# Kernel tuning notes

Measured on AMD Instinct MI355X. Metric: run time of the kernel, lower is better.

Reference implementation:

```python
import jax, jax.numpy as jnp
import numpy as np

DISCOUNT = 0.95
THRESHOLD = 1e-3


def _make_w(n_actions=8):
    # Deterministic transition stencils from VIN.__init__
    left = [[1, 0], [0, 0], [0, 1], [2, 0], [0, 2], [2, 1], [2, 2], [1, 2]]
    center = [[0, 0], [0, 1], [0, 2], [1, 0], [1, 2], [2, 0], [2, 1], [2, 2]]
    right = [[0, 1], [0, 2], [1, 2], [0, 0], [2, 2], [1, 0], [2, 0], [2, 1]]
    w = np.zeros((n_actions, 1, 3, 3), dtype=np.float32)
    for i in range(n_actions):
        w[i, 0, left[i][0], left[i][1]] = 0.1
        w[i, 0, center[i][0], center[i][1]] = 0.8
        w[i, 0, right[i][0], right[i][1]] = 0.1
    return jnp.asarray(w)


def setup_inputs() -> dict:
    key = jax.random.key(0)
    # reward map (B,1,H,W); scaled so VI converges in a realistic # of iterations
    r = jax.random.normal(key, (8, 1, 256, 256), dtype=jnp.float32) * 0.1
    return {"r": r, "w": _make_w()}


def _conv(x, w):
    # F.conv2d(x, w, stride=1, padding=1) -> NCHW / OIHW, SAME padding for 3x3
    return jax.lax.conv_general_dilated(
        x, w, window_strides=(1, 1), padding="SAME",
        dimension_numbers=("NCHW", "OIHW", "NCHW"))


def reference(r, w):
    """value_iteration_manual: returns (v, policy, q)."""
    thresh = jnp.asarray(THRESHOLD, r.dtype)

    def eval_q(v):
        return _conv(r + v * DISCOUNT, w)  # (B, A, H, W)

    def cond(state):
        _, delta = state
        return delta > thresh

    def body(state):
        v, _ = state
        q = eval_q(v)
        new_v = jnp.max(q, axis=1, keepdims=True)  # (B,1,H,W)
        delta = jnp.max(jnp.abs(new_v - v))
        return new_v, delta

    v0 = jnp.zeros_like(r)
    v, _ = jax.lax.while_loop(cond, body, (v0, jnp.asarray(jnp.inf, r.dtype)))

    q = eval_q(v)
    policy = jax.nn.softmax(q, axis=1)  # exp(q - max) / sum, numerically stable
    return v, policy, q
```

## Files before the change

kernel.cpp:

```cpp
#include <hip/hip_runtime.h>

#define HH 256
#define WW 256
#define PLANE (HH * WW)
#define NB 8
#define NCELL (NB * PLANE)
#define RDIM 66
#define RST 72
#define LCOFF 3
#define SST 67

template<int CTRL>
__device__ __forceinline__ float dpp_old(float oldv, float x) {
    return __int_as_float(__builtin_amdgcn_update_dpp(
        __float_as_int(oldv), __float_as_int(x), CTRL, 0xf, 0xf, false));
}

__device__ __forceinline__ float dpp_left(float x) {
    return __int_as_float(__builtin_amdgcn_update_dpp(
        0, __float_as_int(x), 0x111, 0xf, 0xf, true));
}
__device__ __forceinline__ float dpp_right(float x) {
    return __int_as_float(__builtin_amdgcn_update_dpp(
        0, __float_as_int(x), 0x101, 0xf, 0xf, true));
}

template<bool FIRST, bool OUTV>
__global__ __launch_bounds__(1024, 8) void vi_cols(
    const float* __restrict__ r, const float* __restrict__ xin,
    float* __restrict__ xout)
{
    __shared__ float Xs[66 * SST];
    __shared__ float ebuf[2 * 16 * 2 * 64];
    __shared__ float Ts[32 * 33];

    const int blk = blockIdx.x;
    const int b = blk >> 6, ty = (blk >> 3) & 7, tx = blk & 7;
    const int gy0 = ty * 32 - 17, gx0 = tx * 32 - 17;
    const float* rbp = r + b * PLANE;
    const float* xb = xin + b * PLANE;

    for (int idx = threadIdx.x; idx < 66 * 66; idx += 1024) {
        int rr_ = idx / 66, rc = idx - rr_ * 66;
        int py = gy0 + rr_, px = gx0 + rc;
        float xv = 0.f;
        if ((unsigned)py < HH && (unsigned)px < WW) {
            int gi = py * WW + px;
            xv = FIRST ? rbp[gi] : xb[gi];
        }
        Xs[rr_ * SST + rc] = xv;
    }
    __syncthreads();

    const int w = threadIdx.x >> 6;
    const int l = threadIdx.x & 63;
    const int c0 = 4 * w;
    const int py = gy0 + 1 + l;
    const bool rowin = ((unsigned)py < HH);
    const int pxg = gx0 + c0 + 1;
    const bool grpin = ((unsigned)pxg <= (unsigned)(WW - 4));
    const bool act = rowin && grpin;

    float x[6], rt[6], rbo[6];
#pragma unroll
    for (int c = 0; c < 6; ++c) {
        x[c]   = Xs[(1 + l) * SST + c0 + c];
        rt[c]  = Xs[0 * SST + c0 + c];
        rbo[c] = Xs[65 * SST + c0 + c];
    }

    float rr[5];
    {
        float4 ra = make_float4(0.f, 0.f, 0.f, 0.f);
        if (act) ra = *(const float4*)(rbp + py * WW + pxg);
        rr[1] = ra.x; rr[2] = ra.y; rr[3] = ra.z; rr[4] = ra.w;
    }

    const int eb_w0 = (w * 2 + 0) * 64 + l;
    const int eb_w1 = (w * 2 + 1) * 64 + l;
    const int eb_rl = (w > 0)  ? (((w - 1) * 2 + 1) * 64 + l) : 0;
    const int eb_rr = (w < 15) ? (((w + 1) * 2 + 0) * 64 + l) : 0;
    const int PSTRIDE = 16 * 2 * 64;
    const int swl = 4 * w + 3;
    const int swr = 63 - 4 * w;
    const int sLim = min(16, min(swl, swr));

    for (int s = 0; s < 16; ++s) {
        const int po = (s & 1) * PSTRIDE;
        if (s < sLim) {
            float U[6], D[6];
#pragma unroll
            for (int c = 0; c < 6; ++c) {
                U[c] = dpp_old<0x138>(rt[c], x[c]);
                D[c] = dpp_old<0x130>(rbo[c], x[c]);
            }
            float pA = fmaf(8.f, U[0], x[0]);
            float qA = fmaf(8.f, D[0], x[0]);
            float vA = fmaf(8.f, x[0], U[0] + D[0]);
            float pB = fmaf(8.f, U[1], x[1]);
            float qB = fmaf(8.f, D[1], x[1]);
            float vB = fmaf(8.f, x[1], U[1] + D[1]);
            float nx[5];
#pragma unroll
            for (int c = 1; c <= 4; ++c) {
                float pC = fmaf(8.f, U[c + 1], x[c + 1]);
                float qC = fmaf(8.f, D[c + 1], x[c + 1]);
                float vC = fmaf(8.f, x[c + 1], U[c + 1] + D[c + 1]);
                float hT = fmaf(8.f, U[c], U[c - 1] + U[c + 1]);
                float hB = fmaf(8.f, D[c], D[c - 1] + D[c + 1]);
                float t0 = pA + U[c];
                float t2 = pC + U[c];
                float t5 = qA + D[c];
                float t7 = qC + D[c];
                float m1 = fmaxf(fmaxf(t0, hT), t2);
                float m2 = fmaxf(fmaxf(vA, vC), t5);
                float m3 = fmaxf(fmaxf(m1, m2), hB);
                float m  = fmaxf(m3, t7);
                nx[c] = act ? fmaf(0.095f, m, rr[c]) : 0.f;
                pA = pB; pB = pC; qA = qB; qB = qC; vA = vB; vB = vC;
            }
#pragma unroll
            for (int c = 1; c <= 4; ++c) x[c] = nx[c];
            ebuf[po + eb_w0] = x[1];
            ebuf[po + eb_w1] = x[4];
        }
        __syncthreads();
        if (s < sLim) {
            if (w > 0)  x[0] = ebuf[po + eb_rl];
            if (w < 15) x[5] = ebuf[po + eb_rr];
        }
    }

    if (w >= 4 && w <= 11 && l >= 16 && l < 48) {
        const int trow = l - 16;
#pragma unroll
        for (int c = 1; c <= 4; ++c) {
            int tcol = c0 + c - 17;
            float v = OUTV ? (x[c] - rr[c]) * (1.0f / 0.95f) : x[c];
            Ts[trow * 33 + tcol] = v;
        }
    }
    __syncthreads();
    {
        int i = threadIdx.x;
        int trow = i >> 5, tcol = i & 31;
        xout[b * PLANE + (gy0 + 17 + trow) * WW + (gx0 + 17 + tcol)] =
            Ts[trow * 33 + tcol];
    }
}

struct R6 { float v[6]; };

__device__ __forceinline__ R6 load_row(const float* __restrict__ xin,
                                       int base, int lc0, int g) {
    float4 m = *(const float4*)(xin + base + lc0);
    float lf = dpp_left(m.w);
    float rt = dpp_right(m.x);
    if (g == 0)  lf = xin[base + lc0 - 1];
    if (g == 15) rt = xin[base + lc0 + 4];
    R6 o;
    o.v[0] = lf; o.v[1] = m.x; o.v[2] = m.y; o.v[3] = m.z; o.v[4] = m.w; o.v[5] = rt;
    return o;
}

__device__ __forceinline__ float4 step4(const R6& T, const R6& M, const R6& B) {
    float P[6], Q[6], V[6];
#pragma unroll
    for (int j = 0; j < 6; ++j) {
        P[j] = fmaf(8.f, T.v[j], M.v[j]);
        Q[j] = fmaf(8.f, B.v[j], M.v[j]);
        V[j] = fmaf(8.f, M.v[j], T.v[j] + B.v[j]);
    }
    float out[4];
#pragma unroll
    for (int k = 0; k < 4; ++k) {
        float hT = fmaf(8.f, T.v[k + 1], T.v[k] + T.v[k + 2]);
        float hB = fmaf(8.f, B.v[k + 1], B.v[k] + B.v[k + 2]);
        float t0 = P[k] + T.v[k + 1];
        float t2 = P[k + 2] + T.v[k + 1];
        float t5 = Q[k] + B.v[k + 1];
        float t7 = Q[k + 2] + B.v[k + 1];
        float m1 = fmaxf(fmaxf(t0, hT), t2);
        float m2 = fmaxf(fmaxf(V[k], V[k + 2]), t5);
        float m3 = fmaxf(fmaxf(m1, m2), hB);
        out[k] = fmaxf(m3, t7);
    }
    return make_float4(out[0], out[1], out[2], out[3]);
}

__device__ __forceinline__ void t8f(const float* T, const float* M, const float* B,
                                    float t[8]) {
    t[0] = fmaf(8.f, T[0], M[0] + T[1]);
    t[1] = fmaf(8.f, T[1], T[0] + T[2]);
    t[2] = fmaf(8.f, T[2], T[1] + M[2]);
    t[3] = fmaf(8.f, M[0], B[0] + T[0]);
    t[4] = fmaf(8.f, M[2], T[2] + B[2]);
    t[5] = fmaf(8.f, B[0], B[1] + M[0]);
    t[6] = fmaf(8.f, B[1], B[2] + B[0]);
    t[7] = fmaf(8.f, B[2], M[2] + B[1]);
}

__device__ __forceinline__ float maxt(const float t[8]) {
    float m1 = fmaxf(fmaxf(t[0], t[1]), t[2]);
    float m2 = fmaxf(fmaxf(t[3], t[4]), t[5]);
    float m3 = fmaxf(fmaxf(m1, m2), t[6]);
    return fmaxf(m3, t[7]);
}

__device__ __forceinline__ float4 fmaf4(float4 m, float4 rr) {
    return make_float4(fmaf(0.095f, m.x, rr.x), fmaf(0.095f, m.y, rr.y),
                       fmaf(0.095f, m.z, rr.z), fmaf(0.095f, m.w, rr.w));
}

__device__ __forceinline__ void final_row(const R6& T, const R6& M, const R6& B,
                                          int b, int py, int px0,
                                          float* __restrict__ vout,
                                          float* __restrict__ qout,
                                          float* __restrict__ pout) {
    float v4[4], qv[8][4], pv[8][4];
#pragma unroll
    for (int k = 0; k < 4; ++k) {
        float t[8];
        t8f(T.v + k, M.v + k, B.v + k, t);
        float m = maxt(t);
        v4[k] = 0.1f * m;
        float e[8], s = 0.f;
#pragma unroll
        for (int a = 0; a < 8; ++a) { e[a] = __expf(0.1f * (t[a] - m)); s += e[a]; }
        float inv = 1.0f / s;
#pragma unroll
        for (int a = 0; a < 8; ++a) { qv[a][k] = 0.1f * t[a]; pv[a][k] = e[a] * inv; }
    }
    int ob = b * PLANE + py * WW + px0;
    *(float4*)(vout + ob) = make_float4(v4[0], v4[1], v4[2], v4[3]);
    int qb = b * 8 * PLANE + py * WW + px0;
#pragma unroll
    for (int a = 0; a < 8; ++a) {
        *(float4*)(qout + qb + a * PLANE) = make_float4(qv[a][0], qv[a][1], qv[a][2], qv[a][3]);
        *(float4*)(pout + qb + a * PLANE) = make_float4(pv[a][0], pv[a][1], pv[a][2], pv[a][3]);
    }
}

__global__ __launch_bounds__(512, 4) void vi_last(
    const float* __restrict__ r, const float* __restrict__ xin,
    float* __restrict__ vout, float* __restrict__ qout, float* __restrict__ pout)
{
    __shared__ __align__(16) float X[2][RDIM * RST];
    const int blk = blockIdx.x;
    const int b = blk >> 6, ty = (blk >> 3) & 7, tx = blk & 7;
    const int gy0 = ty * 32 - 17, gx0 = tx * 32 - 17;
    const float* rb = r + b * PLANE;
    const float* xb = xin + b * PLANE;

    for (int idx = threadIdx.x; idx < RDIM * RDIM; idx += 512) {
        int rr = idx / RDIM, rc = idx - rr * RDIM;
        int py = gy0 + rr, px = gx0 + rc;
        float val = 0.f;
        if ((unsigned)py < HH && (unsigned)px < WW)
            val = xb[py * WW + px];
        int lidx = rr * RST + rc + LCOFF;
        X[0][lidx] = val;
        X[1][lidx] = val;
    }

    const int g = threadIdx.x & 15;
    const int strip = threadIdx.x >> 4;
    const int wv = threadIdx.x >> 6;
    const int lc0 = 4 + 4 * g;
    const int rr0 = 1 + 2 * strip;
    const int px0 = gx0 + lc0 - LCOFF;
    const bool colin = ((unsigned)px0 < WW);
    const int py0 = gy0 + rr0;
    const bool row0in = ((unsigned)py0 < HH);
    const bool row1in = ((unsigned)(py0 + 1) < HH);

    float4 r0 = make_float4(0.f, 0.f, 0.f, 0.f), r1 = r0;
    if (colin && row0in) r0 = *(const float4*)(rb + py0 * WW + px0);
    if (colin && row1in) r1 = *(const float4*)(rb + (py0 + 1) * WW + px0);

    __syncthreads();

    const bool edge_wave = (wv == 0) | (wv == 7);
    const int base0 = (rr0 - 1) * RST;
    for (int s = 0; s < 15; ++s) {
        const float* xs = X[s & 1];
        float* xo = X[(s & 1) ^ 1];
        if (!(edge_wave && s >= 8)) {
            R6 A = load_row(xs, base0, lc0, g);
            R6 B = load_row(xs, base0 + RST, lc0, g);
            R6 C = load_row(xs, base0 + 2 * RST, lc0, g);
            float4 o0 = step4(A, B, C);
            R6 D = load_row(xs, base0 + 3 * RST, lc0, g);
            float4 o1 = step4(B, C, D);
            if (colin) {
                if (row0in) *(float4*)(xo + base0 + RST + lc0) = fmaf4(o0, r0);
                if (row1in) *(float4*)(xo + base0 + 2 * RST + lc0) = fmaf4(o1, r1);
            }
        }
        __syncthreads();
    }

    if (wv >= 2 && wv <= 5) {
        const float* xf = X[1];
        R6 A = load_row(xf, base0, lc0, g);
        R6 B = load_row(xf, base0 + RST, lc0, g);
        R6 C = load_row(xf, base0 + 2 * RST, lc0, g);
        R6 D = load_row(xf, base0 + 3 * RST, lc0, g);
        if (g >= 4 && g <= 11) {
            final_row(A, B, C, b, py0, px0, vout, qout, pout);
            final_row(B, C, D, b, py0 + 1, px0, vout, qout, pout);
        }
    }
}

__global__ __launch_bounds__(256) void vi_final(const float* __restrict__ r,
                                                const float* __restrict__ v,
                                                float* __restrict__ qout,
                                                float* __restrict__ pout) {
    int c = blockIdx.x * 256 + threadIdx.x;
    int x = c & (WW - 1);
    int y = (c >> 8) & (HH - 1);
    int b = c >> 16;
    float xin[9];
#pragma unroll
    for (int dy = -1; dy <= 1; ++dy)
#pragma unroll
        for (int dx = -1; dx <= 1; ++dx) {
            int yy = y + dy, xx = x + dx;
            float val = 0.0f;
            if ((unsigned)yy < HH && (unsigned)xx < WW)
                val = fmaf(0.95f, v[c + dy * WW + dx], r[c + dy * WW + dx]);
            xin[(dy + 1) * 3 + (dx + 1)] = val;
        }
    constexpr int Lt[8] = {3, 0, 1, 6, 2, 7, 8, 5};
    constexpr int Ct[8] = {0, 1, 2, 3, 5, 6, 7, 8};
    constexpr int Rt[8] = {1, 2, 5, 0, 8, 3, 6, 7};
    float q[8];
#pragma unroll
    for (int a = 0; a < 8; ++a) {
        float t = 0.1f * xin[Lt[a]];
        t = fmaf(0.8f, xin[Ct[a]], t);
        t = fmaf(0.1f, xin[Rt[a]], t);
        q[a] = t;
    }
    float m = q[0];
#pragma unroll
    for (int a = 1; a < 8; ++a) m = fmaxf(m, q[a]);
    float e[8], s = 0.f;
#pragma unroll
    for (int a = 0; a < 8; ++a) { e[a] = __expf(q[a] - m); s += e[a]; }
    float inv = 1.0f / s;
    int basec = b * (8 * PLANE) + (c & (PLANE - 1));
#pragma unroll
    for (int a = 0; a < 8; ++a) {
        qout[basec + a * PLANE] = q[a];
        pout[basec + a * PLANE] = e[a] * inv;
    }
}

extern "C" void kernel_launch(void* const* d_in, const int* in_sizes, int n_in,
                              void* d_out, int out_size, void* d_ws, size_t ws_size,
                              hipStream_t stream) {
    const float* r = (const float*)d_in[0];
    float* out = (float*)d_out;
    float* vslot = out;
    float* pol   = out + NCELL;
    float* qslot = out + 9 * NCELL;

    if (ws_size >= (size_t)(2 * NCELL * sizeof(float))) {
        float* w0 = (float*)d_ws;
        float* w1 = w0 + NCELL;
        vi_cols<true,  false><<<512, 1024, 0, stream>>>(r, nullptr, w0);
        vi_cols<false, false><<<512, 1024, 0, stream>>>(r, w0, w1);
        vi_cols<false, false><<<512, 1024, 0, stream>>>(r, w1, w0);
        vi_cols<false, false><<<512, 1024, 0, stream>>>(r, w0, w1);
        vi_cols<false, false><<<512, 1024, 0, stream>>>(r, w1, w0);
        vi_last<<<512, 512, 0, stream>>>(r, w0, vslot, qslot, pol);
    } else {
        vi_cols<true,  false><<<512, 1024, 0, stream>>>(r, nullptr, pol);
        vi_cols<false, false><<<512, 1024, 0, stream>>>(r, pol, qslot);
        vi_cols<false, false><<<512, 1024, 0, stream>>>(r, qslot, pol);
        vi_cols<false, false><<<512, 1024, 0, stream>>>(r, pol, qslot);
        vi_cols<false, false><<<512, 1024, 0, stream>>>(r, qslot, pol);
        vi_cols<false, true ><<<512, 1024, 0, stream>>>(r, pol, vslot);
        vi_final<<<NCELL / 256, 256, 0, stream>>>(r, vslot, qslot, pol);
    }
}
```

Baseline: 139.5 us.

## Rebuild final VI kernel on register-column DPP scheme with staged coalesced outputs

```diff
diff --git a/kernel.cpp b/kernel.cpp
--- a/kernel.cpp
+++ b/kernel.cpp
@@ -5,9 +5,6 @@
 #define PLANE (HH * WW)
 #define NB 8
 #define NCELL (NB * PLANE)
-#define RDIM 66
-#define RST 72
-#define LCOFF 3
 #define SST 67
 
 template<int CTRL>
@@ -16,14 +13,42 @@
         __float_as_int(oldv), __float_as_int(x), CTRL, 0xf, 0xf, false));
 }
 
-__device__ __forceinline__ float dpp_left(float x) {
-    return __int_as_float(__builtin_amdgcn_update_dpp(
-        0, __float_as_int(x), 0x111, 0xf, 0xf, true));
-}
-__device__ __forceinline__ float dpp_right(float x) {
-    return __int_as_float(__builtin_amdgcn_update_dpp(
-        0, __float_as_int(x), 0x101, 0xf, 0xf, true));
-}
+__device__ __forceinline__ void t8f(const float* T, const float* M, const float* B,
+                                    float t[8]) {
+    t[0] = fmaf(8.f, T[0], M[0] + T[1]);
+    t[1] = fmaf(8.f, T[1], T[0] + T[2]);
+    t[2] = fmaf(8.f, T[2], T[1] + M[2]);
+    t[3] = fmaf(8.f, M[0], B[0] + T[0]);
+    t[4] = fmaf(8.f, M[2], T[2] + B[2]);
+    t[5] = fmaf(8.f, B[0], B[1] + M[0]);
+    t[6] = fmaf(8.f, B[1], B[2] + B[0]);
+    t[7] = fmaf(8.f, B[2], M[2] + B[1]);
+}
+__device__ __forceinline__ float maxt(const float t[8]) {
+    float m1 = fmaxf(fmaxf(t[0], t[1]), t[2]);
+    float m2 = fmaxf(fmaxf(t[3], t[4]), t[5]);
+    float m3 = fmaxf(fmaxf(m1, m2), t[6]);
+    return fmaxf(m3, t[7]);
+}
+template<int A>
+__device__ __forceinline__ float tap1(const float* U, const float* x,
+                                      const float* D, int c) {
+    if (A == 0) return fmaf(8.f, U[c - 1], x[c - 1] + U[c]);
+    if (A == 1) return fmaf(8.f, U[c],     U[c - 1] + U[c + 1]);
+    if (A == 2) return fmaf(8.f, U[c + 1], U[c] + x[c + 1]);
+    if (A == 3) return fmaf(8.f, x[c - 1], D[c - 1] + U[c - 1]);
+    if (A == 4) return fmaf(8.f, x[c + 1], U[c + 1] + D[c + 1]);
+    if (A == 5) return fmaf(8.f, D[c - 1], D[c] + x[c - 1]);
+    if (A == 6) return fmaf(8.f, D[c],     D[c + 1] + D[c - 1]);
+    return fmaf(8.f, D[c + 1], x[c + 1] + D[c]);
+}
+
+#define DECODE_BLK() \
+    const int blk = blockIdx.x; \
+    const int b = blk & 7; \
+    const int tile = blk >> 3; \
+    const int ty = tile >> 3, tx = tile & 7; \
+    const int gy0 = ty * 32 - 17, gx0 = tx * 32 - 17;
 
 template<bool FIRST, bool OUTV>
 __global__ __launch_bounds__(1024, 8) void vi_cols(
@@ -34,9 +59,7 @@
     __shared__ float ebuf[2 * 16 * 2 * 64];
     __shared__ float Ts[32 * 33];
 
-    const int blk = blockIdx.x;
-    const int b = blk >> 6, ty = (blk >> 3) & 7, tx = blk & 7;
-    const int gy0 = ty * 32 - 17, gx0 = tx * 32 - 17;
+    DECODE_BLK();
     const float* rbp = r + b * PLANE;
     const float* xb = xin + b * PLANE;
 
@@ -68,7 +91,6 @@
         rt[c]  = Xs[0 * SST + c0 + c];
         rbo[c] = Xs[65 * SST + c0 + c];
     }
-
     float rr[5];
     {
         float4 ra = make_float4(0.f, 0.f, 0.f, 0.f);
@@ -81,9 +103,7 @@
     const int eb_rl = (w > 0)  ? (((w - 1) * 2 + 1) * 64 + l) : 0;
     const int eb_rr = (w < 15) ? (((w + 1) * 2 + 0) * 64 + l) : 0;
     const int PSTRIDE = 16 * 2 * 64;
-    const int swl = 4 * w + 3;
-    const int swr = 63 - 4 * w;
-    const int sLim = min(16, min(swl, swr));
+    const int sLim = min(16, min(4 * w + 3, 63 - 4 * w));
 
     for (int s = 0; s < 16; ++s) {
         const int po = (s & 1) * PSTRIDE;
@@ -149,167 +169,163 @@
     }
 }
 
-struct R6 { float v[6]; };
-
-__device__ __forceinline__ R6 load_row(const float* __restrict__ xin,
-                                       int base, int lc0, int g) {
-    float4 m = *(const float4*)(xin + base + lc0);
-    float lf = dpp_left(m.w);
-    float rt = dpp_right(m.x);
-    if (g == 0)  lf = xin[base + lc0 - 1];
-    if (g == 15) rt = xin[base + lc0 + 4];
-    R6 o;
-    o.v[0] = lf; o.v[1] = m.x; o.v[2] = m.y; o.v[3] = m.z; o.v[4] = m.w; o.v[5] = rt;
-    return o;
-}
-
-__device__ __forceinline__ float4 step4(const R6& T, const R6& M, const R6& B) {
-    float P[6], Q[6], V[6];
-#pragma unroll
-    for (int j = 0; j < 6; ++j) {
-        P[j] = fmaf(8.f, T.v[j], M.v[j]);
-        Q[j] = fmaf(8.f, B.v[j], M.v[j]);
-        V[j] = fmaf(8.f, M.v[j], T.v[j] + B.v[j]);
-    }
-    float out[4];
-#pragma unroll
-    for (int k = 0; k < 4; ++k) {
-        float hT = fmaf(8.f, T.v[k + 1], T.v[k] + T.v[k + 2]);
-        float hB = fmaf(8.f, B.v[k + 1], B.v[k] + B.v[k + 2]);
-        float t0 = P[k] + T.v[k + 1];
-        float t2 = P[k + 2] + T.v[k + 1];
-        float t5 = Q[k] + B.v[k + 1];
-        float t7 = Q[k + 2] + B.v[k + 1];
-        float m1 = fmaxf(fmaxf(t0, hT), t2);
-        float m2 = fmaxf(fmaxf(V[k], V[k + 2]), t5);
-        float m3 = fmaxf(fmaxf(m1, m2), hB);
-        out[k] = fmaxf(m3, t7);
-    }
-    return make_float4(out[0], out[1], out[2], out[3]);
-}
-
-__device__ __forceinline__ void t8f(const float* T, const float* M, const float* B,
-                                    float t[8]) {
-    t[0] = fmaf(8.f, T[0], M[0] + T[1]);
-    t[1] = fmaf(8.f, T[1], T[0] + T[2]);
-    t[2] = fmaf(8.f, T[2], T[1] + M[2]);
-    t[3] = fmaf(8.f, M[0], B[0] + T[0]);
-    t[4] = fmaf(8.f, M[2], T[2] + B[2]);
-    t[5] = fmaf(8.f, B[0], B[1] + M[0]);
-    t[6] = fmaf(8.f, B[1], B[2] + B[0]);
-    t[7] = fmaf(8.f, B[2], M[2] + B[1]);
-}
-
-__device__ __forceinline__ float maxt(const float t[8]) {
-    float m1 = fmaxf(fmaxf(t[0], t[1]), t[2]);
-    float m2 = fmaxf(fmaxf(t[3], t[4]), t[5]);
-    float m3 = fmaxf(fmaxf(m1, m2), t[6]);
-    return fmaxf(m3, t[7]);
-}
-
-__device__ __forceinline__ float4 fmaf4(float4 m, float4 rr) {
-    return make_float4(fmaf(0.095f, m.x, rr.x), fmaf(0.095f, m.y, rr.y),
-                       fmaf(0.095f, m.z, rr.z), fmaf(0.095f, m.w, rr.w));
-}
-
-__device__ __forceinline__ void final_row(const R6& T, const R6& M, const R6& B,
-                                          int b, int py, int px0,
-                                          float* __restrict__ vout,
-                                          float* __restrict__ qout,
-                                          float* __restrict__ pout) {
-    float v4[4], qv[8][4], pv[8][4];
-#pragma unroll
-    for (int k = 0; k < 4; ++k) {
-        float t[8];
-        t8f(T.v + k, M.v + k, B.v + k, t);
-        float m = maxt(t);
-        v4[k] = 0.1f * m;
-        float e[8], s = 0.f;
-#pragma unroll
-        for (int a = 0; a < 8; ++a) { e[a] = __expf(0.1f * (t[a] - m)); s += e[a]; }
-        float inv = 1.0f / s;
-#pragma unroll
-        for (int a = 0; a < 8; ++a) { qv[a][k] = 0.1f * t[a]; pv[a][k] = e[a] * inv; }
-    }
-    int ob = b * PLANE + py * WW + px0;
-    *(float4*)(vout + ob) = make_float4(v4[0], v4[1], v4[2], v4[3]);
-    int qb = b * 8 * PLANE + py * WW + px0;
-#pragma unroll
-    for (int a = 0; a < 8; ++a) {
-        *(float4*)(qout + qb + a * PLANE) = make_float4(qv[a][0], qv[a][1], qv[a][2], qv[a][3]);
-        *(float4*)(pout + qb + a * PLANE) = make_float4(pv[a][0], pv[a][1], pv[a][2], pv[a][3]);
-    }
-}
-
-__global__ __launch_bounds__(512, 4) void vi_last(
+__global__ __launch_bounds__(1024, 8) void vi_cols_last(
     const float* __restrict__ r, const float* __restrict__ xin,
     float* __restrict__ vout, float* __restrict__ qout, float* __restrict__ pout)
 {
-    __shared__ __align__(16) float X[2][RDIM * RST];
-    const int blk = blockIdx.x;
-    const int b = blk >> 6, ty = (blk >> 3) & 7, tx = blk & 7;
-    const int gy0 = ty * 32 - 17, gx0 = tx * 32 - 17;
-    const float* rb = r + b * PLANE;
+    __shared__ float Xs[66 * SST];
+    __shared__ float ebuf[2 * 16 * 2 * 64];
+    __shared__ float TsA[32 * 33];
+    __shared__ float TsB[32 * 33];
+
+    DECODE_BLK();
+    const float* rbp = r + b * PLANE;
     const float* xb = xin + b * PLANE;
 
-    for (int idx = threadIdx.x; idx < RDIM * RDIM; idx += 512) {
-        int rr = idx / RDIM, rc = idx - rr * RDIM;
-        int py = gy0 + rr, px = gx0 + rc;
-        float val = 0.f;
+    for (int idx = threadIdx.x; idx < 66 * 66; idx += 1024) {
+        int rr_ = idx / 66, rc = idx - rr_ * 66;
+        int py = gy0 + rr_, px = gx0 + rc;
+        float xv = 0.f;
         if ((unsigned)py < HH && (unsigned)px < WW)
-            val = xb[py * WW + px];
-        int lidx = rr * RST + rc + LCOFF;
-        X[0][lidx] = val;
-        X[1][lidx] = val;
-    }
-
-    const int g = threadIdx.x & 15;
-    const int strip = threadIdx.x >> 4;
-    const int wv = threadIdx.x >> 6;
-    const int lc0 = 4 + 4 * g;
-    const int rr0 = 1 + 2 * strip;
-    const int px0 = gx0 + lc0 - LCOFF;
-    const bool colin = ((unsigned)px0 < WW);
-    const int py0 = gy0 + rr0;
-    const bool row0in = ((unsigned)py0 < HH);
-    const bool row1in = ((unsigned)(py0 + 1) < HH);
-
-    float4 r0 = make_float4(0.f, 0.f, 0.f, 0.f), r1 = r0;
-    if (colin && row0in) r0 = *(const float4*)(rb + py0 * WW + px0);
-    if (colin && row1in) r1 = *(const float4*)(rb + (py0 + 1) * WW + px0);
-
+            xv = xb[py * WW + px];
+        Xs[rr_ * SST + rc] = xv;
+    }
     __syncthreads();
 
-    const bool edge_wave = (wv == 0) | (wv == 7);
-    const int base0 = (rr0 - 1) * RST;
+    const int w = threadIdx.x >> 6;
+    const int l = threadIdx.x & 63;
+    const int c0 = 4 * w;
+    const int py = gy0 + 1 + l;
+    const bool rowin = ((unsigned)py < HH);
+    const int pxg = gx0 + c0 + 1;
+    const bool grpin = ((unsigned)pxg <= (unsigned)(WW - 4));
+    const bool act = rowin && grpin;
+
+    float x[6], rt[6], rbo[6];
+#pragma unroll
+    for (int c = 0; c < 6; ++c) {
+        x[c]   = Xs[(1 + l) * SST + c0 + c];
+        rt[c]  = Xs[0 * SST + c0 + c];
+        rbo[c] = Xs[65 * SST + c0 + c];
+    }
+    float rr[5];
+    {
+        float4 ra = make_float4(0.f, 0.f, 0.f, 0.f);
+        if (act) ra = *(const float4*)(rbp + py * WW + pxg);
+        rr[1] = ra.x; rr[2] = ra.y; rr[3] = ra.z; rr[4] = ra.w;
+    }
+
+    const int eb_w0 = (w * 2 + 0) * 64 + l;
+    const int eb_w1 = (w * 2 + 1) * 64 + l;
+    const int eb_rl = (w > 0)  ? (((w - 1) * 2 + 1) * 64 + l) : 0;
+    const int eb_rr = (w < 15) ? (((w + 1) * 2 + 0) * 64 + l) : 0;
+    const int PSTRIDE = 16 * 2 * 64;
+    const int sLim = min(16, min(4 * w + 3, 63 - 4 * w));
+
     for (int s = 0; s < 15; ++s) {
-        const float* xs = X[s & 1];
-        float* xo = X[(s & 1) ^ 1];
-        if (!(edge_wave && s >= 8)) {
-            R6 A = load_row(xs, base0, lc0, g);
-            R6 B = load_row(xs, base0 + RST, lc0, g);
-            R6 C = load_row(xs, base0 + 2 * RST, lc0, g);
-            float4 o0 = step4(A, B, C);
-            R6 D = load_row(xs, base0 + 3 * RST, lc0, g);
-            float4 o1 = step4(B, C, D);
-            if (colin) {
-                if (row0in) *(float4*)(xo + base0 + RST + lc0) = fmaf4(o0, r0);
-                if (row1in) *(float4*)(xo + base0 + 2 * RST + lc0) = fmaf4(o1, r1);
+        const int po = (s & 1) * PSTRIDE;
+        if (s < sLim) {
+            float U[6], D[6];
+#pragma unroll
+            for (int c = 0; c < 6; ++c) {
+                U[c] = dpp_old<0x138>(rt[c], x[c]);
+                D[c] = dpp_old<0x130>(rbo[c], x[c]);
             }
+            float pA = fmaf(8.f, U[0], x[0]);
+            float qA = fmaf(8.f, D[0], x[0]);
+            float vA = fmaf(8.f, x[0], U[0] + D[0]);
+            float pB = fmaf(8.f, U[1], x[1]);
+            float qB = fmaf(8.f, D[1], x[1]);
+            float vB = fmaf(8.f, x[1], U[1] + D[1]);
+            float nx[5];
+#pragma unroll
+            for (int c = 1; c <= 4; ++c) {
+                float pC = fmaf(8.f, U[c + 1], x[c + 1]);
+                float qC = fmaf(8.f, D[c + 1], x[c + 1]);
+                float vC = fmaf(8.f, x[c + 1], U[c + 1] + D[c + 1]);
+                float hT = fmaf(8.f, U[c], U[c - 1] + U[c + 1]);
+                float hB = fmaf(8.f, D[c], D[c - 1] + D[c + 1]);
+                float t0 = pA + U[c];
+                float t2 = pC + U[c];
+                float t5 = qA + D[c];
+                float t7 = qC + D[c];
+                float m1 = fmaxf(fmaxf(t0, hT), t2);
+                float m2 = fmaxf(fmaxf(vA, vC), t5);
+                float m3 = fmaxf(fmaxf(m1, m2), hB);
+                float m  = fmaxf(m3, t7);
+                nx[c] = act ? fmaf(0.095f, m, rr[c]) : 0.f;
+                pA = pB; pB = pC; qA = qB; qB = qC; vA = vB; vB = vC;
+            }
+#pragma unroll
+            for (int c = 1; c <= 4; ++c) x[c] = nx[c];
+            ebuf[po + eb_w0] = x[1];
+            ebuf[po + eb_w1] = x[4];
         }
         __syncthreads();
-    }
-
-    if (wv >= 2 && wv <= 5) {
-        const float* xf = X[1];
-        R6 A = load_row(xf, base0, lc0, g);
-        R6 B = load_row(xf, base0 + RST, lc0, g);
-        R6 C = load_row(xf, base0 + 2 * RST, lc0, g);
-        R6 D = load_row(xf, base0 + 3 * RST, lc0, g);
-        if (g >= 4 && g <= 11) {
-            final_row(A, B, C, b, py0, px0, vout, qout, pout);
-            final_row(B, C, D, b, py0 + 1, px0, vout, qout, pout);
-        }
+        if (s < sLim) {
+            if (w > 0)  x[0] = ebuf[po + eb_rl];
+            if (w < 15) x[5] = ebuf[po + eb_rr];
+        }
+    }
+
+    float U[6], D[6];
+#pragma unroll
+    for (int c = 0; c < 6; ++c) {
+        U[c] = dpp_old<0x138>(rt[c], x[c]);
+        D[c] = dpp_old<0x130>(rbo[c], x[c]);
+    }
+    const bool center = (w >= 4 && w <= 11) && (l >= 16 && l < 48);
+    float m4[4], is4[4];
+#pragma unroll
+    for (int c = 1; c <= 4; ++c) {
+        float t[8];
+        t8f(U + (c - 1), x + (c - 1), D + (c - 1), t);
+        float m = maxt(t);
+        float s = 0.f;
+#pragma unroll
+        for (int a = 0; a < 8; ++a) s += __expf(0.1f * (t[a] - m));
+        m4[c - 1] = m;
+        is4[c - 1] = 1.0f / s;
+    }
+
+    const int trow = l - 16;
+    const int i = threadIdx.x;
+    const int orow = i >> 5, ocol = i & 31;
+    const int obase = (gy0 + 17 + orow) * WW + (gx0 + 17 + ocol);
+
+    if (center) {
+#pragma unroll
+        for (int c = 1; c <= 4; ++c)
+            TsA[trow * 33 + (c0 + c - 17)] = 0.1f * m4[c - 1];
+    }
+    __syncthreads();
+    vout[b * PLANE + obase] = TsA[orow * 33 + ocol];
+
+#pragma unroll
+    for (int a = 0; a < 8; ++a) {
+        __syncthreads();
+        if (center) {
+#pragma unroll
+            for (int c = 1; c <= 4; ++c) {
+                float t;
+                switch (a) {
+                case 0: t = tap1<0>(U, x, D, c); break;
+                case 1: t = tap1<1>(U, x, D, c); break;
+                case 2: t = tap1<2>(U, x, D, c); break;
+                case 3: t = tap1<3>(U, x, D, c); break;
+                case 4: t = tap1<4>(U, x, D, c); break;
+                case 5: t = tap1<5>(U, x, D, c); break;
+                case 6: t = tap1<6>(U, x, D, c); break;
+                default: t = tap1<7>(U, x, D, c); break;
+                }
+                TsA[trow * 33 + (c0 + c - 17)] = 0.1f * t;
+                TsB[trow * 33 + (c0 + c - 17)] =
+                    __expf(0.1f * (t - m4[c - 1])) * is4[c - 1];
+            }
+        }
+        __syncthreads();
+        qout[b * 8 * PLANE + a * PLANE + obase] = TsA[orow * 33 + ocol];
+        pout[b * 8 * PLANE + a * PLANE + obase] = TsB[orow * 33 + ocol];
     }
 }
 
@@ -375,7 +391,7 @@
         vi_cols<false, false><<<512, 1024, 0, stream>>>(r, w1, w0);
         vi_cols<false, false><<<512, 1024, 0, stream>>>(r, w0, w1);
         vi_cols<false, false><<<512, 1024, 0, stream>>>(r, w1, w0);
-        vi_last<<<512, 512, 0, stream>>>(r, w0, vslot, qslot, pol);
+        vi_cols_last<<<512, 1024, 0, stream>>>(r, w0, vslot, qslot, pol);
     } else {
         vi_cols<true,  false><<<512, 1024, 0, stream>>>(r, nullptr, pol);
         vi_cols<false, false><<<512, 1024, 0, stream>>>(r, pol, qslot);
```

Result: no change. 137.4 us (-1.6%).
